# Kernel optimization log

Hardware: AMD Instinct MI355X
Metric: run time of the kernel (lower is better)

Reference implementation:

```python
import jax, jax.numpy as jnp
import numpy as np

EMB = 256  # embedding_dim


def setup_inputs() -> dict:
    key = jax.random.key(0)
    k1, k2, k3 = jax.random.split(key, 3)
    B, P, N, D = 32, 4, 1024, EMB
    x = jax.random.normal(k1, (B, P, N, D), dtype=jnp.float32)
    W_qkv = jax.random.normal(k2, (D, 1 + 2 * D), dtype=jnp.float32) * (1.0 / np.sqrt(D))
    b_qkv = jnp.zeros((1 + 2 * D,), dtype=jnp.float32)
    W_o = jax.random.normal(k3, (D, D), dtype=jnp.float32) * (1.0 / np.sqrt(D))
    b_o = jnp.zeros((D,), dtype=jnp.float32)
    return {"x": x, "W_qkv": W_qkv, "b_qkv": b_qkv, "W_o": W_o, "b_o": b_o}


def reference(x, W_qkv, b_qkv, W_o, b_o):
    # x: [B, P, N, D]
    D = W_o.shape[0]
    qkv = jnp.einsum('bpnd,de->bpne', x, W_qkv) + b_qkv  # [B,P,N,1+2D]
    q = qkv[..., :1]                 # [B,P,N,1]
    k = qkv[..., 1:1 + D]            # [B,P,N,D]
    v = jax.nn.relu(qkv[..., 1 + D:])  # [B,P,N,D]
    # softmax over the patch axis N (axis=2)
    context_scores = jax.nn.softmax(q, axis=2)  # [B,P,N,1]
    # dropout layers operate in inference mode here (identity)
    context_vector = jnp.sum(k * context_scores, axis=2, keepdims=True)  # [B,P,1,D]
    updated_values = v * context_vector  # broadcast multiply, [B,P,N,D]
    final = jnp.einsum('bpnd,de->bpne', updated_values, W_o) + b_o  # [B,P,N,D]
    return final
```

## Files before the change

kernel.cpp:

```cpp
#include <hip/hip_runtime.h>


typedef float  floatx4 __attribute__((ext_vector_type(4)));
typedef __bf16 bf16x8  __attribute__((ext_vector_type(8)));
typedef unsigned short u16;
typedef u16 u16x8 __attribute__((ext_vector_type(8)));

#define NGRP 128

__device__ __forceinline__ float bf2f(u16 u) {
    union { unsigned int i; float f; } c; c.i = ((unsigned int)u) << 16; return c.f;
}
__device__ __forceinline__ u16 f2bf(float f) {
    union { __bf16 h; u16 u; } c; c.h = (__bf16)f; return c.u;
}
__device__ __forceinline__ floatx4 mfma16(bf16x8 a, bf16x8 b, floatx4 c) {
    return __builtin_amdgcn_mfma_f32_16x16x32_bf16(a, b, c, 0, 0, 0);
}

__global__ __launch_bounds__(256) void k_prep(
    const float* __restrict__ Wqkv, const float* __restrict__ Wo,
    u16* __restrict__ Wqkv_p, u16* __restrict__ Wo_p,
    float* __restrict__ wqp, float* __restrict__ cvu, float* __restrict__ Sg)
{
    const int i = blockIdx.x * 256 + threadIdx.x;
    if (i < 32 * 4096) {
        const int j = i & 7, lane = (i >> 3) & 63, kk = (i >> 9) & 7, ct = i >> 12;
        const int k = kk * 32 + (lane >> 4) * 8 + j;
        Wqkv_p[i] = f2bf(Wqkv[k * 513 + (1 + ct * 16 + (lane & 15))]);
    }
    if (i < 16 * 4096) {
        const int j = i & 7, lane = (i >> 3) & 63, kk = (i >> 9) & 7, ct = i >> 12;
        const int k = kk * 32 + (lane >> 4) * 8 + j;
        Wo_p[i] = f2bf(Wo[k * 256 + (ct * 16 + (lane & 15))]);
    }
    if (i < 256) wqp[i] = Wqkv[i * 513];
    if (i < NGRP * 256) cvu[i] = 0.f;
    if (i < NGRP) Sg[i] = 0.f;
}

__global__ __launch_bounds__(512, 4) void k_qkv(
    const float* __restrict__ x, const u16* __restrict__ Wp,
    const float* __restrict__ wqp, const float* __restrict__ bqkv,
    u16* __restrict__ Vw, float* __restrict__ cvu, float* __restrict__ Sg)
{
    const int tid = threadIdx.x;
    const int w = tid >> 6, lane = tid & 63, quad = lane >> 4, n16 = lane & 15;
    const int m0 = blockIdx.x * 64;
    const int g  = blockIdx.x >> 4;

    __shared__ u16 As[64 * 256];
    __shared__ float e_s[64];

#pragma unroll
    for (int it = 0; it < 4; it++) {
        const int c = it * 512 + tid;
        const int row = c >> 5, col = c & 31;
        const float* xp = x + (size_t)(m0 + row) * 256 + col * 8;
        floatx4 u0 = *(const floatx4*)xp;
        floatx4 u1 = *(const floatx4*)(xp + 4);
        u16x8 o;
        o[0] = f2bf(u0[0]); o[1] = f2bf(u0[1]); o[2] = f2bf(u0[2]); o[3] = f2bf(u0[3]);
        o[4] = f2bf(u1[0]); o[5] = f2bf(u1[1]); o[6] = f2bf(u1[2]); o[7] = f2bf(u1[3]);
        *(u16x8*)(As + row * 256 + ((col ^ (row & 15)) * 8)) = o;
    }
    __syncthreads();

    {
        const int r = tid >> 3, s = tid & 7;
        float qacc = 0.f;
#pragma unroll
        for (int j = 0; j < 4; j++) {
            const int c = s * 4 + j;
            u16x8 xv = *(const u16x8*)(As + r * 256 + ((c ^ (r & 15)) * 8));
            floatx4 w0 = *(const floatx4*)(wqp + c * 8);
            floatx4 w1 = *(const floatx4*)(wqp + c * 8 + 4);
            qacc += bf2f(xv[0]) * w0[0] + bf2f(xv[1]) * w0[1]
                  + bf2f(xv[2]) * w0[2] + bf2f(xv[3]) * w0[3]
                  + bf2f(xv[4]) * w1[0] + bf2f(xv[5]) * w1[1]
                  + bf2f(xv[6]) * w1[2] + bf2f(xv[7]) * w1[3];
        }
        qacc += __shfl_xor(qacc, 1, 64);
        qacc += __shfl_xor(qacc, 2, 64);
        qacc += __shfl_xor(qacc, 4, 64);
        if (s == 0) e_s[r] = __expf(qacc + bqkv[0]);
    }
    __syncthreads();

    floatx4 acc[4][4];
#pragma unroll
    for (int i = 0; i < 4; i++)
#pragma unroll
        for (int rt = 0; rt < 4; rt++) acc[i][rt] = (floatx4){0.f, 0.f, 0.f, 0.f};

#pragma unroll
    for (int kk = 0; kk < 8; kk++) {
        bf16x8 a[4];
#pragma unroll
        for (int rt = 0; rt < 4; rt++) {
            const int row = rt * 16 + n16;
            a[rt] = __builtin_bit_cast(bf16x8,
                *(const u16x8*)(As + row * 256 + (((kk * 4 + quad) ^ n16) * 8)));
        }
#pragma unroll
        for (int i = 0; i < 4; i++) {
            const int ct = w + 8 * i;
            bf16x8 b = __builtin_bit_cast(bf16x8,
                *(const u16x8*)(Wp + (size_t)((ct * 8 + kk) * 64 + lane) * 8));
#pragma unroll
            for (int rt = 0; rt < 4; rt++) acc[i][rt] = mfma16(a[rt], b, acc[i][rt]);
        }
    }

    if (tid < 64) {
        float e = e_s[tid];
#pragma unroll
        for (int s = 32; s > 0; s >>= 1) e += __shfl_xor(e, s, 64);
        if (tid == 0) atomicAdd(Sg + g, e);
    }

#pragma unroll
    for (int i = 0; i < 2; i++) {
        const int c = (w + 8 * i) * 16 + n16;
        const float bias = bqkv[1 + c];
        float p = 0.f;
#pragma unroll
        for (int rt = 0; rt < 4; rt++)
#pragma unroll
            for (int r = 0; r < 4; r++)
                p += e_s[rt * 16 + quad * 4 + r] * (acc[i][rt][r] + bias);
        p += __shfl_xor(p, 16, 64);
        p += __shfl_xor(p, 32, 64);
        if (lane < 16) atomicAdd(cvu + g * 256 + c, p);
    }

#pragma unroll
    for (int i = 2; i < 4; i++) {
        const int cfull = (w + 8 * i) * 16 + n16;
        const float bias = bqkv[1 + cfull];
        const int cvn = cfull - 256;
#pragma unroll
        for (int rt = 0; rt < 4; rt++) {
            const int rowb = m0 + rt * 16 + quad * 4;
#pragma unroll
            for (int r = 0; r < 4; r++)
                Vw[(size_t)(rowb + r) * 256 + cvn] = f2bf(fmaxf(acc[i][rt][r] + bias, 0.f));
        }
    }
}

__global__ __launch_bounds__(512, 4) void k_out(
    const u16* __restrict__ Vw, const u16* __restrict__ Wop,
    const float* __restrict__ cvu, const float* __restrict__ Sg,
    const float* __restrict__ bo, float* __restrict__ out)
{
    const int tid = threadIdx.x;
    const int w = tid >> 6, lane = tid & 63, quad = lane >> 4, n16 = lane & 15;
    const int m0 = blockIdx.x * 64;
    const int g  = blockIdx.x >> 4;

    __shared__ u16 Vs[64 * 256];
    __shared__ float cvs[256];

    if (tid < 256) cvs[tid] = cvu[g * 256 + tid] * (1.0f / Sg[g]);

#pragma unroll
    for (int it = 0; it < 4; it++) {
        const int c = it * 512 + tid;
        const int row = c >> 5, col = c & 31;
        u16x8 v = *(const u16x8*)(Vw + (size_t)(m0 + row) * 256 + col * 8);
        *(u16x8*)(Vs + row * 256 + ((col ^ (row & 15)) * 8)) = v;
    }
    __syncthreads();

    floatx4 acc[2][4];
#pragma unroll
    for (int i = 0; i < 2; i++)
#pragma unroll
        for (int rt = 0; rt < 4; rt++) acc[i][rt] = (floatx4){0.f, 0.f, 0.f, 0.f};

#pragma unroll
    for (int kk = 0; kk < 8; kk++) {
        bf16x8 a[4];
#pragma unroll
        for (int rt = 0; rt < 4; rt++) {
            const int row = rt * 16 + n16;
            a[rt] = __builtin_bit_cast(bf16x8,
                *(const u16x8*)(Vs + row * 256 + (((kk * 4 + quad) ^ n16) * 8)));
        }
        const floatx4 c0 = *(const floatx4*)(cvs + kk * 32 + quad * 8);
        const floatx4 c1 = *(const floatx4*)(cvs + kk * 32 + quad * 8 + 4);
#pragma unroll
        for (int i = 0; i < 2; i++) {
            const int ct = w + 8 * i;
            u16x8 wo = *(const u16x8*)(Wop + (size_t)((ct * 8 + kk) * 64 + lane) * 8);
            bf16x8 b;
            b[0] = (__bf16)(c0[0] * bf2f(wo[0]));
            b[1] = (__bf16)(c0[1] * bf2f(wo[1]));
            b[2] = (__bf16)(c0[2] * bf2f(wo[2]));
            b[3] = (__bf16)(c0[3] * bf2f(wo[3]));
            b[4] = (__bf16)(c1[0] * bf2f(wo[4]));
            b[5] = (__bf16)(c1[1] * bf2f(wo[5]));
            b[6] = (__bf16)(c1[2] * bf2f(wo[6]));
            b[7] = (__bf16)(c1[3] * bf2f(wo[7]));
#pragma unroll
            for (int rt = 0; rt < 4; rt++) acc[i][rt] = mfma16(a[rt], b, acc[i][rt]);
        }
    }

#pragma unroll
    for (int i = 0; i < 2; i++) {
        const int c = (w + 8 * i) * 16 + n16;
        const float bias = bo[c];
#pragma unroll
        for (int rt = 0; rt < 4; rt++) {
            const int rowb = m0 + rt * 16 + quad * 4;
#pragma unroll
            for (int r = 0; r < 4; r++)
                out[(size_t)(rowb + r) * 256 + c] = acc[i][rt][r] + bias;
        }
    }
}

extern "C" void kernel_launch(void* const* d_in, const int* in_sizes, int n_in,
                              void* d_out, int out_size, void* d_ws, size_t ws_size,
                              hipStream_t stream)
{
    const float* x    = (const float*)d_in[0];
    const float* Wqkv = (const float*)d_in[1];
    const float* bqkv = (const float*)d_in[2];
    const float* Wo   = (const float*)d_in[3];
    const float* bo   = (const float*)d_in[4];
    float* out = (float*)d_out;

    char* ws = (char*)d_ws;
    u16*   Vw    = (u16*)(ws);
    u16*   Wqkvp = (u16*)(ws + 67108864);
    u16*   Wop   = (u16*)(ws + 67371008);
    float* wqp   = (float*)(ws + 67502080);
    float* cvu   = (float*)(ws + 67503104);
    float* Sg    = (float*)(ws + 67634176);

    k_prep<<<512, 256, 0, stream>>>(Wqkv, Wo, Wqkvp, Wop, wqp, cvu, Sg);
    k_qkv <<<2048, 512, 0, stream>>>(x, Wqkvp, wqp, bqkv, Vw, cvu, Sg);
    k_out <<<2048, 512, 0, stream>>>(Vw, Wop, cvu, Sg, bo, out);
}
```

Measured before the change: 308.8 us.

## Reassociate context vector via softmax-weighted x sum and fuse V and output GEMMs

```diff
diff --git a/kernel.cpp b/kernel.cpp
--- a/kernel.cpp
+++ b/kernel.cpp
@@ -20,29 +20,83 @@
 
 __global__ __launch_bounds__(256) void k_prep(
     const float* __restrict__ Wqkv, const float* __restrict__ Wo,
-    u16* __restrict__ Wqkv_p, u16* __restrict__ Wo_p,
-    float* __restrict__ wqp, float* __restrict__ cvu, float* __restrict__ Sg)
+    u16* __restrict__ Wvp, u16* __restrict__ Wop,
+    float* __restrict__ wqp, float* __restrict__ y, float* __restrict__ Sg)
 {
     const int i = blockIdx.x * 256 + threadIdx.x;
-    if (i < 32 * 4096) {
-        const int j = i & 7, lane = (i >> 3) & 63, kk = (i >> 9) & 7, ct = i >> 12;
-        const int k = kk * 32 + (lane >> 4) * 8 + j;
-        Wqkv_p[i] = f2bf(Wqkv[k * 513 + (1 + ct * 16 + (lane & 15))]);
-    }
-    if (i < 16 * 4096) {
-        const int j = i & 7, lane = (i >> 3) & 63, kk = (i >> 9) & 7, ct = i >> 12;
-        const int k = kk * 32 + (lane >> 4) * 8 + j;
-        Wo_p[i] = f2bf(Wo[k * 256 + (ct * 16 + (lane & 15))]);
-    }
+    const int j = i & 7, lane = (i >> 3) & 63, kk = (i >> 9) & 7, ct = i >> 12;
+    const int k = kk * 32 + (lane >> 4) * 8 + j;
+    Wvp[i] = f2bf(Wqkv[k * 513 + (257 + ct * 16 + (lane & 15))]);
+    Wop[i] = f2bf(Wo[k * 256 + (ct * 16 + (lane & 15))]);
     if (i < 256) wqp[i] = Wqkv[i * 513];
-    if (i < NGRP * 256) cvu[i] = 0.f;
+    if (i < NGRP * 256) y[i] = 0.f;
     if (i < NGRP) Sg[i] = 0.f;
 }
 
-__global__ __launch_bounds__(512, 4) void k_qkv(
-    const float* __restrict__ x, const u16* __restrict__ Wp,
-    const float* __restrict__ wqp, const float* __restrict__ bqkv,
-    u16* __restrict__ Vw, float* __restrict__ cvu, float* __restrict__ Sg)
+__global__ __launch_bounds__(256) void k_sum(
+    const float* __restrict__ x, const float* __restrict__ wqp,
+    const float* __restrict__ bqkv,
+    float* __restrict__ y, float* __restrict__ Sg)
+{
+    const int tid = threadIdx.x;
+    const int m0 = blockIdx.x * 64;
+    const int g  = blockIdx.x >> 4;
+    __shared__ float e_s[64];
+
+    {
+        const int r = tid >> 2, s = tid & 3;
+        const float* xp = x + (size_t)(m0 + r) * 256 + s * 4;
+        const float* wp = wqp + s * 4;
+        float q = 0.f;
+#pragma unroll
+        for (int j = 0; j < 16; j++) {
+            floatx4 xv = *(const floatx4*)(xp + j * 16);
+            floatx4 wv = *(const floatx4*)(wp + j * 16);
+            q += xv[0] * wv[0] + xv[1] * wv[1] + xv[2] * wv[2] + xv[3] * wv[3];
+        }
+        q += __shfl_xor(q, 1, 64);
+        q += __shfl_xor(q, 2, 64);
+        if (s == 0) e_s[r] = __expf(q + bqkv[0]);
+    }
+    __syncthreads();
+
+    if (tid < 64) {
+        float e = e_s[tid];
+#pragma unroll
+        for (int s = 32; s > 0; s >>= 1) e += __shfl_xor(e, s, 64);
+        if (tid == 0) atomicAdd(Sg + g, e);
+    }
+
+    {
+        float acc = 0.f;
+        const float* xp = x + (size_t)m0 * 256 + tid;
+#pragma unroll 8
+        for (int r = 0; r < 64; r++) acc += e_s[r] * xp[r * 256];
+        atomicAdd(y + g * 256 + tid, acc);
+    }
+}
+
+__global__ __launch_bounds__(256) void k_cv(
+    const float* __restrict__ Wqkv, const float* __restrict__ bqkv,
+    const float* __restrict__ y, const float* __restrict__ Sg,
+    float* __restrict__ cv)
+{
+    const int g = blockIdx.x, d = threadIdx.x;
+    __shared__ float ys[256];
+    ys[d] = y[g * 256 + d] * (1.0f / Sg[g]);
+    __syncthreads();
+    float acc = bqkv[1 + d];
+    const float* wp = Wqkv + 1 + d;
+#pragma unroll 4
+    for (int t = 0; t < 256; t++) acc += ys[t] * wp[t * 513];
+    cv[g * 256 + d] = acc;
+}
+
+__global__ __launch_bounds__(512, 4) void k_vo(
+    const float* __restrict__ x, const u16* __restrict__ Wvp,
+    const u16* __restrict__ Wop, const float* __restrict__ cv,
+    const float* __restrict__ bqkv, const float* __restrict__ bo,
+    float* __restrict__ out)
 {
     const int tid = threadIdx.x;
     const int w = tid >> 6, lane = tid & 63, quad = lane >> 4, n16 = lane & 15;
@@ -50,7 +104,9 @@
     const int g  = blockIdx.x >> 4;
 
     __shared__ u16 As[64 * 256];
-    __shared__ float e_s[64];
+    __shared__ float cvs[256];
+
+    if (tid < 256) cvs[tid] = cv[g * 256 + tid];
 
 #pragma unroll
     for (int it = 0; it < 4; it++) {
@@ -66,30 +122,9 @@
     }
     __syncthreads();
 
-    {
-        const int r = tid >> 3, s = tid & 7;
-        float qacc = 0.f;
-#pragma unroll
-        for (int j = 0; j < 4; j++) {
-            const int c = s * 4 + j;
-            u16x8 xv = *(const u16x8*)(As + r * 256 + ((c ^ (r & 15)) * 8));
-            floatx4 w0 = *(const floatx4*)(wqp + c * 8);
-            floatx4 w1 = *(const floatx4*)(wqp + c * 8 + 4);
-            qacc += bf2f(xv[0]) * w0[0] + bf2f(xv[1]) * w0[1]
-                  + bf2f(xv[2]) * w0[2] + bf2f(xv[3]) * w0[3]
-                  + bf2f(xv[4]) * w1[0] + bf2f(xv[5]) * w1[1]
-                  + bf2f(xv[6]) * w1[2] + bf2f(xv[7]) * w1[3];
-        }
-        qacc += __shfl_xor(qacc, 1, 64);
-        qacc += __shfl_xor(qacc, 2, 64);
-        qacc += __shfl_xor(qacc, 4, 64);
-        if (s == 0) e_s[r] = __expf(qacc + bqkv[0]);
-    }
-    __syncthreads();
-
-    floatx4 acc[4][4];
-#pragma unroll
-    for (int i = 0; i < 4; i++)
+    floatx4 acc[2][4];
+#pragma unroll
+    for (int i = 0; i < 2; i++)
 #pragma unroll
         for (int rt = 0; rt < 4; rt++) acc[i][rt] = (floatx4){0.f, 0.f, 0.f, 0.f};
 
@@ -103,81 +138,39 @@
                 *(const u16x8*)(As + row * 256 + (((kk * 4 + quad) ^ n16) * 8)));
         }
 #pragma unroll
-        for (int i = 0; i < 4; i++) {
+        for (int i = 0; i < 2; i++) {
             const int ct = w + 8 * i;
             bf16x8 b = __builtin_bit_cast(bf16x8,
-                *(const u16x8*)(Wp + (size_t)((ct * 8 + kk) * 64 + lane) * 8));
+                *(const u16x8*)(Wvp + (size_t)((ct * 8 + kk) * 64 + lane) * 8));
 #pragma unroll
             for (int rt = 0; rt < 4; rt++) acc[i][rt] = mfma16(a[rt], b, acc[i][rt]);
         }
     }
-
-    if (tid < 64) {
-        float e = e_s[tid];
-#pragma unroll
-        for (int s = 32; s > 0; s >>= 1) e += __shfl_xor(e, s, 64);
-        if (tid == 0) atomicAdd(Sg + g, e);
-    }
+    __syncthreads();
 
 #pragma unroll
     for (int i = 0; i < 2; i++) {
-        const int c = (w + 8 * i) * 16 + n16;
-        const float bias = bqkv[1 + c];
-        float p = 0.f;
-#pragma unroll
-        for (int rt = 0; rt < 4; rt++)
-#pragma unroll
-            for (int r = 0; r < 4; r++)
-                p += e_s[rt * 16 + quad * 4 + r] * (acc[i][rt][r] + bias);
-        p += __shfl_xor(p, 16, 64);
-        p += __shfl_xor(p, 32, 64);
-        if (lane < 16) atomicAdd(cvu + g * 256 + c, p);
-    }
-
-#pragma unroll
-    for (int i = 2; i < 4; i++) {
-        const int cfull = (w + 8 * i) * 16 + n16;
-        const float bias = bqkv[1 + cfull];
-        const int cvn = cfull - 256;
-#pragma unroll
-        for (int rt = 0; rt < 4; rt++) {
-            const int rowb = m0 + rt * 16 + quad * 4;
-#pragma unroll
-            for (int r = 0; r < 4; r++)
-                Vw[(size_t)(rowb + r) * 256 + cvn] = f2bf(fmaxf(acc[i][rt][r] + bias, 0.f));
-        }
-    }
-}
-
-__global__ __launch_bounds__(512, 4) void k_out(
-    const u16* __restrict__ Vw, const u16* __restrict__ Wop,
-    const float* __restrict__ cvu, const float* __restrict__ Sg,
-    const float* __restrict__ bo, float* __restrict__ out)
-{
-    const int tid = threadIdx.x;
-    const int w = tid >> 6, lane = tid & 63, quad = lane >> 4, n16 = lane & 15;
-    const int m0 = blockIdx.x * 64;
-    const int g  = blockIdx.x >> 4;
-
-    __shared__ u16 Vs[64 * 256];
-    __shared__ float cvs[256];
-
-    if (tid < 256) cvs[tid] = cvu[g * 256 + tid] * (1.0f / Sg[g]);
-
-#pragma unroll
-    for (int it = 0; it < 4; it++) {
-        const int c = it * 512 + tid;
-        const int row = c >> 5, col = c & 31;
-        u16x8 v = *(const u16x8*)(Vw + (size_t)(m0 + row) * 256 + col * 8);
-        *(u16x8*)(Vs + row * 256 + ((col ^ (row & 15)) * 8)) = v;
-    }
-    __syncthreads();
-
-    floatx4 acc[2][4];
+        const int col = (w + 8 * i) * 16 + n16;
+        const float bias = bqkv[257 + col];
+        const float scale = cvs[col];
+        const int cc = col >> 3, co = col & 7;
+#pragma unroll
+        for (int rt = 0; rt < 4; rt++) {
+#pragma unroll
+            for (int r = 0; r < 4; r++) {
+                const int row = rt * 16 + quad * 4 + r;
+                const float vv = fmaxf(acc[i][rt][r] + bias, 0.f) * scale;
+                As[row * 256 + ((cc ^ (row & 15)) * 8) + co] = f2bf(vv);
+            }
+        }
+    }
+    __syncthreads();
+
+    floatx4 acc2[2][4];
 #pragma unroll
     for (int i = 0; i < 2; i++)
 #pragma unroll
-        for (int rt = 0; rt < 4; rt++) acc[i][rt] = (floatx4){0.f, 0.f, 0.f, 0.f};
+        for (int rt = 0; rt < 4; rt++) acc2[i][rt] = (floatx4){0.f, 0.f, 0.f, 0.f};
 
 #pragma unroll
     for (int kk = 0; kk < 8; kk++) {
@@ -186,38 +179,28 @@
         for (int rt = 0; rt < 4; rt++) {
             const int row = rt * 16 + n16;
             a[rt] = __builtin_bit_cast(bf16x8,
-                *(const u16x8*)(Vs + row * 256 + (((kk * 4 + quad) ^ n16) * 8)));
-        }
-        const floatx4 c0 = *(const floatx4*)(cvs + kk * 32 + quad * 8);
-        const floatx4 c1 = *(const floatx4*)(cvs + kk * 32 + quad * 8 + 4);
+                *(const u16x8*)(As + row * 256 + (((kk * 4 + quad) ^ n16) * 8)));
+        }
 #pragma unroll
         for (int i = 0; i < 2; i++) {
             const int ct = w + 8 * i;
-            u16x8 wo = *(const u16x8*)(Wop + (size_t)((ct * 8 + kk) * 64 + lane) * 8);
-            bf16x8 b;
-            b[0] = (__bf16)(c0[0] * bf2f(wo[0]));
-            b[1] = (__bf16)(c0[1] * bf2f(wo[1]));
-            b[2] = (__bf16)(c0[2] * bf2f(wo[2]));
-            b[3] = (__bf16)(c0[3] * bf2f(wo[3]));
-            b[4] = (__bf16)(c1[0] * bf2f(wo[4]));
-            b[5] = (__bf16)(c1[1] * bf2f(wo[5]));
-            b[6] = (__bf16)(c1[2] * bf2f(wo[6]));
-            b[7] = (__bf16)(c1[3] * bf2f(wo[7]));
-#pragma unroll
-            for (int rt = 0; rt < 4; rt++) acc[i][rt] = mfma16(a[rt], b, acc[i][rt]);
+            bf16x8 b = __builtin_bit_cast(bf16x8,
+                *(const u16x8*)(Wop + (size_t)((ct * 8 + kk) * 64 + lane) * 8));
+#pragma unroll
+            for (int rt = 0; rt < 4; rt++) acc2[i][rt] = mfma16(a[rt], b, acc2[i][rt]);
         }
     }
 
 #pragma unroll
     for (int i = 0; i < 2; i++) {
-        const int c = (w + 8 * i) * 16 + n16;
-        const float bias = bo[c];
+        const int col = (w + 8 * i) * 16 + n16;
+        const float bias = bo[col];
 #pragma unroll
         for (int rt = 0; rt < 4; rt++) {
             const int rowb = m0 + rt * 16 + quad * 4;
 #pragma unroll
             for (int r = 0; r < 4; r++)
-                out[(size_t)(rowb + r) * 256 + c] = acc[i][rt][r] + bias;
+                out[(size_t)(rowb + r) * 256 + col] = acc2[i][rt][r] + bias;
         }
     }
 }
@@ -234,14 +217,15 @@
     float* out = (float*)d_out;
 
     char* ws = (char*)d_ws;
-    u16*   Vw    = (u16*)(ws);
-    u16*   Wqkvp = (u16*)(ws + 67108864);
-    u16*   Wop   = (u16*)(ws + 67371008);
-    float* wqp   = (float*)(ws + 67502080);
-    float* cvu   = (float*)(ws + 67503104);
-    float* Sg    = (float*)(ws + 67634176);
-
-    k_prep<<<512, 256, 0, stream>>>(Wqkv, Wo, Wqkvp, Wop, wqp, cvu, Sg);
-    k_qkv <<<2048, 512, 0, stream>>>(x, Wqkvp, wqp, bqkv, Vw, cvu, Sg);
-    k_out <<<2048, 512, 0, stream>>>(Vw, Wop, cvu, Sg, bo, out);
-}
+    u16*   Wvp = (u16*)(ws);
+    u16*   Wop = (u16*)(ws + 131072);
+    float* wqp = (float*)(ws + 262144);
+    float* y   = (float*)(ws + 263168);
+    float* Sg  = (float*)(ws + 394240);
+    float* cv  = (float*)(ws + 394752);
+
+    k_prep<<<256,  256, 0, stream>>>(Wqkv, Wo, Wvp, Wop, wqp, y, Sg);
+    k_sum <<<2048, 256, 0, stream>>>(x, wqp, bqkv, y, Sg);
+    k_cv  <<<NGRP, 256, 0, stream>>>(Wqkv, bqkv, y, Sg, cv);
+    k_vo  <<<2048, 512, 0, stream>>>(x, Wvp, Wop, cv, bqkv, bo, out);
+}
```

After: 327.1 us. 1.06x slower.
